# Kernel tuning notes

Hardware: AMD Instinct MI355X
Metric: run time of the kernel (lower is better)

The kernel has to match this reference:

```python
import jax, jax.numpy as jnp
import numpy as np

BRANCH = 8
LEVELS = 7
N = (BRANCH ** LEVELS - 1) // (BRANCH - 1)  # 299593 nodes, complete 8-ary tree
VOCAB, IN_DIM, MEM = 50000, 300, 150


def _tree_structure():
    parent = np.empty(N, np.int32)
    parent[0] = N  # sentinel: root scatters into dropped segment N
    idx = np.arange(1, N)
    parent[1:] = (idx - 1) // BRANCH
    depth = np.empty(N, np.int32)
    start = 0
    for d in range(LEVELS):
        cnt = BRANCH ** d
        depth[start:start + cnt] = d
        start += cnt
    return jnp.asarray(parent), jnp.asarray(depth)


def setup_inputs() -> dict:
    key = jax.random.key(0)
    ks = jax.random.split(key, 20)
    parent, depth = _tree_structure()
    inp = {
        'tokens': jax.random.randint(ks[0], (N,), 0, VOCAB, dtype=jnp.int32),
        'parent': parent,
        'depth': depth,
        'max_depth': LEVELS,
        'emb': jax.random.normal(ks[1], (VOCAB, IN_DIM), jnp.float32) * 0.1,
    }
    names_x = ['Wix', 'Wfx', 'Wox', 'Wux']
    names_h = ['Wih', 'Wfh', 'Woh', 'Wuh']
    sx = 1.0 / np.sqrt(IN_DIM)
    sh = 1.0 / np.sqrt(MEM)
    for j, (nx, nh) in enumerate(zip(names_x, names_h)):
        inp[nx] = jax.random.normal(ks[2 + 4 * j], (MEM, IN_DIM), jnp.float32) * sx
        inp['b' + nx[1:]] = jax.random.normal(ks[3 + 4 * j], (MEM,), jnp.float32) * sx
        inp[nh] = jax.random.normal(ks[4 + 4 * j], (MEM, MEM), jnp.float32) * sh
        inp['b' + nh[1:]] = jax.random.normal(ks[5 + 4 * j], (MEM,), jnp.float32) * sh
    return inp


def reference(tokens, parent, depth, max_depth, emb,
              Wix, bix, Wih, bih, Wfx, bfx, Wfh, bfh,
              Wox, box, Woh, boh, Wux, bux, Wuh, buh):
    n = tokens.shape[0]
    x = emb[tokens]  # [N, in_dim]
    # precompute all input-side gate projections once (batched GEMMs)
    ix_x = x @ Wix.T + bix
    fx_x = x @ Wfx.T + bfx
    ox_x = x @ Wox.T + box
    ux_x = x @ Wux.T + bux
    # parent index safe for gathering (root's sentinel -> 0; its row is masked out)
    gparent = jnp.where(parent >= n, 0, parent)

    h = jnp.zeros((n, MEM), x.dtype)
    c = jnp.zeros((n, MEM), x.dtype)

    # level-synchronous bottom-up sweep (loop over tree depth, not data)
    for d in range(max_depth - 1, -1, -1):
        # per-child forget gate: sigmoid(fh(h_child) + fx(x_parent)) * c_child
        f = jax.nn.sigmoid(h @ Wfh.T + bfh + fx_x[gparent])
        fc_sum = jax.ops.segment_sum(f * c, parent, num_segments=n + 1)[:n]
        h_sum = jax.ops.segment_sum(h, parent, num_segments=n + 1)[:n]
        i = jax.nn.sigmoid(ix_x + h_sum @ Wih.T + bih)
        o = jax.nn.sigmoid(ox_x + h_sum @ Woh.T + boh)
        u = jnp.tanh(ux_x + h_sum @ Wuh.T + buh)
        c_new = i * u + fc_sum
        h_new = o * jnp.tanh(c_new)
        mask = (depth == d)[:, None]
        c = jnp.where(mask, c_new, c)
        h = jnp.where(mask, h_new, h)
    # original returns concatenated cell states (post-order); here indexed by node id
    return c
```

## Files before the change

### kernel.cpp

```cpp
#include <hip/hip_runtime.h>


#define MEMD  150
#define IND   300
#define NINT  37449
#define VOCAB 50000
#define GROW  608
#define FSTR  152

typedef short bf16x8 __attribute__((ext_vector_type(8)));
typedef float f32x16 __attribute__((ext_vector_type(16)));
#define ZERO16 {0,0,0,0,0,0,0,0,0,0,0,0,0,0,0,0}

#define GALL_OFF 0ul
#define HSB_OFF  60800000ul
#define FCS_OFF  72200000ul
#define BPX_OFF  94980000ul
#define BPH_OFF  95380000ul

__device__ __forceinline__ float b2f(unsigned short u) {
    union { unsigned int i; float f; } v; v.i = ((unsigned int)u) << 16; return v.f;
}
__device__ __forceinline__ unsigned short f2b(float f) {
    union { float f; unsigned int i; } v; v.f = f;
    unsigned int x = v.i;
    x += 0x7fffu + ((x >> 16) & 1u);
    return (unsigned short)(x >> 16);
}
__device__ __forceinline__ float sigm(float x) {
    return __builtin_amdgcn_rcpf(1.0f + __expf(-x));
}
__device__ __forceinline__ float tanh_fast(float x) {
    float e = __expf(2.0f * x);
    return 1.0f - 2.0f * __builtin_amdgcn_rcpf(e + 1.0f);
}

__global__ void pack_w(const float* __restrict__ Wix, const float* __restrict__ Wox,
                       const float* __restrict__ Wux, const float* __restrict__ Wfx,
                       const float* __restrict__ Wih, const float* __restrict__ Woh,
                       const float* __restrict__ Wuh, const float* __restrict__ Wfh,
                       unsigned short* __restrict__ bpx, unsigned short* __restrict__ bph)
{
    const int total_x = 4 * 5 * 19 * 512;
    const int total_h = 4 * 5 * 10 * 512;
    for (int i = blockIdx.x * blockDim.x + threadIdx.x; i < total_x + total_h;
         i += gridDim.x * blockDim.x) {
        if (i < total_x) {
            int e = i & 7, lane = (i >> 3) & 63, rest = i >> 9;
            int ks = rest % 19; rest /= 19;
            int nt = rest % 5;  int g = rest / 5;
            int col = nt * 32 + (lane & 31);
            int k = ks * 16 + ((lane >> 5) << 3) + e;
            const float* W = (g == 0) ? Wix : (g == 1) ? Wox : (g == 2) ? Wux : Wfx;
            bpx[i] = f2b((col < MEMD && k < IND) ? W[col * IND + k] : 0.f);
        } else {
            int j = i - total_x;
            int e = j & 7, lane = (j >> 3) & 63, rest = j >> 9;
            int ks = rest % 10; rest /= 10;
            int nt = rest % 5;  int g = rest / 5;
            int col = nt * 32 + (lane & 31);
            int k = ks * 16 + ((lane >> 5) << 3) + e;
            const float* W = (g == 0) ? Wih : (g == 1) ? Woh : (g == 2) ? Wuh : Wfh;
            bph[j] = f2b((col < MEMD && k < MEMD) ? W[col * MEMD + k] : 0.f);
        }
    }
}

__global__ __launch_bounds__(640, 2)
void vocab_gemm(const float* __restrict__ emb,
                const float* __restrict__ bix, const float* __restrict__ bih,
                const float* __restrict__ box_, const float* __restrict__ boh,
                const float* __restrict__ bux, const float* __restrict__ buh,
                const float* __restrict__ bfx, const float* __restrict__ bfh,
                const unsigned short* __restrict__ bpx_u,
                unsigned short* __restrict__ gall)
{
    __shared__ __align__(16) char sm0[40960];
    const int tid = threadIdx.x, lane = tid & 63, w = tid >> 6;
    const int hi = lane >> 5, ln31 = lane & 31;
    const int tile0 = blockIdx.x * 64;
    const int rowsValid = min(64, VOCAB - tile0);
    const int mt = (w >= 5) ? 1 : 0, nt = w - mt * 5;

    for (int i = tid; i < 64 * 40; i += 640) {
        int r = i / 40, q = i % 40;
        int rr = (r < rowsValid) ? r : 0;
        const float* er = emb + (long)(tile0 + rr) * IND;
        float4 v0 = {0.f,0.f,0.f,0.f}, v1 = {0.f,0.f,0.f,0.f};
        if (q < 38) v0 = *(const float4*)(er + q * 8);
        if (q < 37) v1 = *(const float4*)(er + q * 8 + 4);
        bf16x8 p;
        p[0]=(short)f2b(v0.x); p[1]=(short)f2b(v0.y); p[2]=(short)f2b(v0.z); p[3]=(short)f2b(v0.w);
        p[4]=(short)f2b(v1.x); p[5]=(short)f2b(v1.y); p[6]=(short)f2b(v1.z); p[7]=(short)f2b(v1.w);
        *(bf16x8*)(sm0 + r * 640 + ((q * 16) ^ ((r & 7) << 4))) = p;
    }
    __syncthreads();

    const bf16x8* BX = (const bf16x8*)bpx_u;
    const int row = mt * 32 + ln31;
    const int col = nt * 32 + ln31;
    const bool colv = col < MEMD;
    const int cc = colv ? col : 0;
    const float* b1[4] = {bix, box_, bux, bfx};
    const float* b2[4] = {bih, boh, buh, bfh};

    for (int g = 0; g < 4; ++g) {
        f32x16 acc = ZERO16;
        bf16x8 aC = *(const bf16x8*)(sm0 + row * 640 + ((hi * 16) ^ ((row & 7) << 4)));
        bf16x8 bC = BX[((g * 5 + nt) * 19 + 0) * 64 + lane];
        #pragma unroll
        for (int ks = 0; ks < 19; ++ks) {
            bf16x8 aN, bN;
            if (ks < 18) {
                aN = *(const bf16x8*)(sm0 + row * 640 + (((ks + 1) * 32 + hi * 16) ^ ((row & 7) << 4)));
                bN = BX[((g * 5 + nt) * 19 + ks + 1) * 64 + lane];
            }
            acc = __builtin_amdgcn_mfma_f32_32x32x16_bf16(aC, bC, acc, 0, 0, 0);
            aC = aN; bC = bN;
        }
        float bias = colv ? (b1[g][cc] + b2[g][cc]) : 0.f;
        #pragma unroll
        for (int r = 0; r < 16; ++r) {
            int rloc = mt * 32 + (r & 3) + 8 * (r >> 2) + 4 * hi;
            if (rloc < rowsValid && colv)
                gall[(long)(tile0 + rloc) * GROW + col * 4 + g] = f2b(acc[r] + bias);
        }
    }
}

template<bool INTERNAL>
__global__ __launch_bounds__(320, INTERNAL ? 2 : 8)
void level_k(const int* __restrict__ tokens,
             const unsigned short* __restrict__ gall,
             const unsigned short* __restrict__ bph_u,
             unsigned short* __restrict__ hsumb, unsigned short* __restrict__ fcsum,
             float* __restrict__ c_out, int base, int cnt, int writePar)
{
    __shared__ __align__(16) char sm0[INTERNAL ? 24576 : 12288];
    __shared__ int toksL[32];
    __shared__ int ptokL[4];
    const int tid = threadIdx.x, lane = tid & 63, w = tid >> 6;
    const int hi = lane >> 5, ln31 = lane & 31;
    const int tile0 = blockIdx.x * 32;
    const int nodeBase = base + tile0;
    const int rowsValid = INTERNAL ? min(32, cnt - tile0) : 32;
    const int p0 = (nodeBase - 1) >> 3;
    const int nt = w;

    if (tid < 32) toksL[tid] = tokens[nodeBase + ((tid < rowsValid) ? tid : 0)];
    if (writePar && tid < 4) ptokL[tid] = tokens[p0 + tid];
    if (INTERNAL) {
        for (int i = tid; i < 32 * 20; i += 320) {
            int r = i / 20, q = i % 20;
            int rr = (r < rowsValid) ? r : 0;
            bf16x8 v = {0,0,0,0,0,0,0,0};
            if (q < 19)
                v = *(const bf16x8*)(hsumb + (long)(nodeBase + rr) * FSTR + q * 8);
            *(bf16x8*)(sm0 + 12288 + r * 384 + ((q * 16) ^ ((r & 7) << 4))) = v;
        }
    }
    __syncthreads();

    const bf16x8* BH = (const bf16x8*)bph_u;
    const int row = ln31;
    const int col = nt * 32 + ln31;
    const bool colv = col < MEMD;
    const int cc = colv ? col : 0;

    f32x16 ai = ZERO16, ao = ZERO16, au = ZERO16;
    if (INTERNAL) {
        const char* hb = sm0 + 12288;
        bf16x8 aC = *(const bf16x8*)(hb + row * 384 + ((hi * 16) ^ ((row & 7) << 4)));
        bf16x8 b0C = BH[((0 * 5 + nt) * 10 + 0) * 64 + lane];
        bf16x8 b1C = BH[((1 * 5 + nt) * 10 + 0) * 64 + lane];
        bf16x8 b2C = BH[((2 * 5 + nt) * 10 + 0) * 64 + lane];
        #pragma unroll
        for (int ks = 0; ks < 10; ++ks) {
            bf16x8 aN, b0N, b1N, b2N;
            if (ks < 9) {
                aN  = *(const bf16x8*)(hb + row * 384 + (((ks + 1) * 32 + hi * 16) ^ ((row & 7) << 4)));
                b0N = BH[((0 * 5 + nt) * 10 + ks + 1) * 64 + lane];
                b1N = BH[((1 * 5 + nt) * 10 + ks + 1) * 64 + lane];
                b2N = BH[((2 * 5 + nt) * 10 + ks + 1) * 64 + lane];
            }
            ai = __builtin_amdgcn_mfma_f32_32x32x16_bf16(aC, b0C, ai, 0, 0, 0);
            ao = __builtin_amdgcn_mfma_f32_32x32x16_bf16(aC, b1C, ao, 0, 0, 0);
            au = __builtin_amdgcn_mfma_f32_32x32x16_bf16(aC, b2C, au, 0, 0, 0);
            aC = aN; b0C = b0N; b1C = b1N; b2C = b2N;
        }
    }

    float cvv[16];
    {
        float hp[4] = {0.f, 0.f, 0.f, 0.f};
        #pragma unroll
        for (int r = 0; r < 16; ++r) {
            int rloc = (r & 3) + 8 * (r >> 2) + 4 * hi;
            bool rv = INTERNAL ? (rloc < rowsValid) : true;
            ushort4 gv = *(const ushort4*)(gall + (long)toksL[rloc] * GROW + cc * 4);
            float fc = 0.f;
            if (INTERNAL) fc = (rv && colv) ? b2f(fcsum[(long)(nodeBase + rloc) * FSTR + col]) : 0.f;
            float iv = sigm((INTERNAL ? ai[r] : 0.f) + b2f(gv.x));
            float ov = sigm((INTERNAL ? ao[r] : 0.f) + b2f(gv.y));
            float uv = tanh_fast((INTERNAL ? au[r] : 0.f) + b2f(gv.z));
            float cv = iv * uv + fc;
            float h = (rv && colv) ? ov * tanh_fast(cv) : 0.f;
            cvv[r] = (rv && colv) ? cv : 0.f;
            if (rv && colv) c_out[(long)(nodeBase + rloc) * MEMD + col] = cv;
            *(unsigned short*)(sm0 + rloc * 384 + ((col * 2) ^ ((rloc & 7) << 4))) = f2b(h);
            hp[r >> 2] += h;
        }
        if (writePar) {
            #pragma unroll
            for (int o = 0; o < 4; ++o) {
                float s = hp[o] + __shfl_xor(hp[o], 32);
                if (lane < 32 && colv && (INTERNAL ? (o * 8 < rowsValid) : true))
                    hsumb[(long)(p0 + o) * FSTR + col] = f2b(s);
            }
        }
    }
    __syncthreads();

    if (writePar) {
        f32x16 ff = ZERO16;
        {
            bf16x8 aC = *(const bf16x8*)(sm0 + row * 384 + ((hi * 16) ^ ((row & 7) << 4)));
            bf16x8 bC = BH[((15 + nt) * 10 + 0) * 64 + lane];
            #pragma unroll
            for (int ks = 0; ks < 10; ++ks) {
                bf16x8 aN, bN;
                if (ks < 9) {
                    aN = *(const bf16x8*)(sm0 + row * 384 + (((ks + 1) * 32 + hi * 16) ^ ((row & 7) << 4)));
                    bN = BH[((15 + nt) * 10 + ks + 1) * 64 + lane];
                }
                ff = __builtin_amdgcn_mfma_f32_32x32x16_bf16(aC, bC, ff, 0, 0, 0);
                aC = aN; bC = bN;
            }
        }
        #pragma unroll
        for (int o = 0; o < 4; ++o) {
            float fx = b2f(gall[(long)ptokL[o] * GROW + cc * 4 + 3]);
            float fp = 0.f;
            #pragma unroll
            for (int q = 0; q < 4; ++q) {
                int r = o * 4 + q;
                fp += sigm(ff[r] + fx) * cvv[r];
            }
            float s = fp + __shfl_xor(fp, 32);
            if (lane < 32 && colv && (INTERNAL ? (o * 8 < rowsValid) : true))
                fcsum[(long)(p0 + o) * FSTR + col] = f2b(s);
        }
    }
}

__global__ __launch_bounds__(320, 2)
void tail_k(const int* __restrict__ tokens,
            const unsigned short* __restrict__ gall,
            const unsigned short* __restrict__ bph_u,
            unsigned short* __restrict__ hsumb, unsigned short* __restrict__ fcsum,
            float* __restrict__ c_out)
{
    __shared__ __align__(16) char sm0[24576];
    __shared__ int toksL[32];
    __shared__ int ptokL[4];
    const int tid = threadIdx.x, lane = tid & 63, w = tid >> 6;
    const int hi = lane >> 5, ln31 = lane & 31;
    const int nt = w;
    const bf16x8* BH = (const bf16x8*)bph_u;
    const int row = ln31;
    const int col = nt * 32 + ln31;
    const bool colv = col < MEMD;
    const int cc = colv ? col : 0;

    const int basesL[3] = {9, 1, 0};
    const int cntsL[3]  = {64, 8, 1};
    const int wpL[3]    = {1, 1, 0};

    for (int li = 0; li < 3; ++li) {
        for (int t0 = 0; t0 < cntsL[li]; t0 += 32) {
            const int nodeBase = basesL[li] + t0;
            const int rowsValid = min(32, cntsL[li] - t0);
            const int p0 = (nodeBase - 1) >> 3;
            const int writePar = wpL[li];

            if (tid < 32) toksL[tid] = tokens[nodeBase + ((tid < rowsValid) ? tid : 0)];
            if (writePar && tid < 4) ptokL[tid] = tokens[p0 + tid];
            for (int i = tid; i < 32 * 20; i += 320) {
                int r = i / 20, q = i % 20;
                int rr = (r < rowsValid) ? r : 0;
                bf16x8 v = {0,0,0,0,0,0,0,0};
                if (q < 19)
                    v = *(const bf16x8*)(hsumb + (long)(nodeBase + rr) * FSTR + q * 8);
                *(bf16x8*)(sm0 + 12288 + r * 384 + ((q * 16) ^ ((r & 7) << 4))) = v;
            }
            __syncthreads();

            f32x16 ai = ZERO16, ao = ZERO16, au = ZERO16;
            {
                const char* hb = sm0 + 12288;
                #pragma unroll
                for (int ks = 0; ks < 10; ++ks) {
                    bf16x8 a = *(const bf16x8*)(hb + row * 384 + ((ks * 32 + hi * 16) ^ ((row & 7) << 4)));
                    ai = __builtin_amdgcn_mfma_f32_32x32x16_bf16(a, BH[((0 * 5 + nt) * 10 + ks) * 64 + lane], ai, 0, 0, 0);
                    ao = __builtin_amdgcn_mfma_f32_32x32x16_bf16(a, BH[((1 * 5 + nt) * 10 + ks) * 64 + lane], ao, 0, 0, 0);
                    au = __builtin_amdgcn_mfma_f32_32x32x16_bf16(a, BH[((2 * 5 + nt) * 10 + ks) * 64 + lane], au, 0, 0, 0);
                }
            }

            float cvv[16];
            {
                float hp[4] = {0.f, 0.f, 0.f, 0.f};
                #pragma unroll
                for (int r = 0; r < 16; ++r) {
                    int rloc = (r & 3) + 8 * (r >> 2) + 4 * hi;
                    bool rv = rloc < rowsValid;
                    ushort4 gv = *(const ushort4*)(gall + (long)toksL[rloc] * GROW + cc * 4);
                    float fc = (rv && colv) ? b2f(fcsum[(long)(nodeBase + rloc) * FSTR + col]) : 0.f;
                    float iv = sigm(ai[r] + b2f(gv.x));
                    float ov = sigm(ao[r] + b2f(gv.y));
                    float uv = tanh_fast(au[r] + b2f(gv.z));
                    float cv = iv * uv + fc;
                    float h = (rv && colv) ? ov * tanh_fast(cv) : 0.f;
                    cvv[r] = (rv && colv) ? cv : 0.f;
                    if (rv && colv) c_out[(long)(nodeBase + rloc) * MEMD + col] = cv;
                    *(unsigned short*)(sm0 + rloc * 384 + ((col * 2) ^ ((rloc & 7) << 4))) = f2b(h);
                    hp[r >> 2] += h;
                }
                if (writePar) {
                    #pragma unroll
                    for (int o = 0; o < 4; ++o) {
                        float s = hp[o] + __shfl_xor(hp[o], 32);
                        if (lane < 32 && colv && o * 8 < rowsValid)
                            hsumb[(long)(p0 + o) * FSTR + col] = f2b(s);
                    }
                }
            }
            __syncthreads();

            if (writePar) {
                f32x16 ff = ZERO16;
                #pragma unroll
                for (int ks = 0; ks < 10; ++ks) {
                    bf16x8 a = *(const bf16x8*)(sm0 + row * 384 + ((ks * 32 + hi * 16) ^ ((row & 7) << 4)));
                    ff = __builtin_amdgcn_mfma_f32_32x32x16_bf16(a, BH[((15 + nt) * 10 + ks) * 64 + lane], ff, 0, 0, 0);
                }
                #pragma unroll
                for (int o = 0; o < 4; ++o) {
                    float fx = b2f(gall[(long)ptokL[o] * GROW + cc * 4 + 3]);
                    float fp = 0.f;
                    #pragma unroll
                    for (int q = 0; q < 4; ++q)
                        fp += sigm(ff[o * 4 + q] + fx) * cvv[o * 4 + q];
                    float s = fp + __shfl_xor(fp, 32);
                    if (lane < 32 && colv && o * 8 < rowsValid)
                        fcsum[(long)(p0 + o) * FSTR + col] = f2b(s);
                }
            }
            __syncthreads();
        }
    }
}

extern "C" void kernel_launch(void* const* d_in, const int* in_sizes, int n_in,
                              void* d_out, int out_size, void* d_ws, size_t ws_size,
                              hipStream_t stream) {
    const int*   tokens = (const int*)d_in[0];
    const float* emb = (const float*)d_in[4];
    const float* Wix = (const float*)d_in[5];  const float* bix = (const float*)d_in[6];
    const float* Wih = (const float*)d_in[7];  const float* bih = (const float*)d_in[8];
    const float* Wfx = (const float*)d_in[9];  const float* bfx = (const float*)d_in[10];
    const float* Wfh = (const float*)d_in[11]; const float* bfh = (const float*)d_in[12];
    const float* Wox = (const float*)d_in[13]; const float* box_ = (const float*)d_in[14];
    const float* Woh = (const float*)d_in[15]; const float* boh = (const float*)d_in[16];
    const float* Wux = (const float*)d_in[17]; const float* bux = (const float*)d_in[18];
    const float* Wuh = (const float*)d_in[19]; const float* buh = (const float*)d_in[20];
    float* c_out = (float*)d_out;
    char* ws = (char*)d_ws;

    unsigned short* gall  = (unsigned short*)(ws + GALL_OFF);
    unsigned short* hsumb = (unsigned short*)(ws + HSB_OFF);
    unsigned short* fcs   = (unsigned short*)(ws + FCS_OFF);
    unsigned short* bpx   = (unsigned short*)(ws + BPX_OFF);
    unsigned short* bph   = (unsigned short*)(ws + BPH_OFF);

    pack_w<<<128, 512, 0, stream>>>(Wix, Wox, Wux, Wfx, Wih, Woh, Wuh, Wfh, bpx, bph);
    vocab_gemm<<<(VOCAB + 63) / 64, 640, 0, stream>>>(
        emb, bix, bih, box_, boh, bux, buh, bfx, bfh, bpx, gall);

    static const int bases[7] = {0, 1, 9, 73, 585, 4681, 37449};
    static const int cnts[7]  = {1, 8, 64, 512, 4096, 32768, 262144};

    level_k<false><<<cnts[6] / 32, 320, 0, stream>>>(
        tokens, gall, bph, hsumb, fcs, c_out, bases[6], cnts[6], 1);
    for (int d = 5; d >= 3; --d) {
        int grid = (cnts[d] + 31) / 32;
        level_k<true><<<grid, 320, 0, stream>>>(
            tokens, gall, bph, hsumb, fcs, c_out, bases[d], cnts[d], 1);
    }
    tail_k<<<1, 320, 0, stream>>>(tokens, gall, bph, hsumb, fcs, c_out);
}
```

Baseline: 302.9 us.

## Precompute leaf hidden states and forget projections per vocab token

Leaf nodes depend only on their token, so leaf h and the Wfh·h projection are computed once per vocabulary entry (50000 rows) rather than per leaf node (262144). They are stored in an fp8 e4m3 table and gathered by a new leaf_csum kernel that reduces the eight children per parent. This removes the per-leaf MFMA GEMM but adds two extra kernels plus fp8 quantisation error in the forget-gate input. Gall stride shrinks from 608 to 600.

```diff
diff --git a/kernel.cpp b/kernel.cpp
--- a/kernel.cpp
+++ b/kernel.cpp
@@ -5,7 +5,7 @@
 #define IND   300
 #define NINT  37449
 #define VOCAB 50000
-#define GROW  608
+#define GROW  600
 #define FSTR  152
 
 typedef short bf16x8 __attribute__((ext_vector_type(8)));
@@ -13,10 +13,11 @@
 #define ZERO16 {0,0,0,0,0,0,0,0,0,0,0,0,0,0,0,0}
 
 #define GALL_OFF 0ul
-#define HSB_OFF  60800000ul
-#define FCS_OFF  72200000ul
-#define BPX_OFF  94980000ul
-#define BPH_OFF  95380000ul
+#define FHX_OFF  60000000ul
+#define HSB_OFF  67600000ul
+#define FCS_OFF  79000000ul
+#define BPX_OFF  90400000ul
+#define BPH_OFF  90800000ul
 
 __device__ __forceinline__ float b2f(unsigned short u) {
     union { unsigned int i; float f; } v; v.i = ((unsigned int)u) << 16; return v.f;
@@ -33,6 +34,34 @@
 __device__ __forceinline__ float tanh_fast(float x) {
     float e = __expf(2.0f * x);
     return 1.0f - 2.0f * __builtin_amdgcn_rcpf(e + 1.0f);
+}
+__device__ __forceinline__ unsigned char f2e4m3(float f) {
+    union { float f; unsigned u; } v; v.f = f;
+    unsigned s = (v.u >> 31) << 7;
+    float af = fabsf(f);
+    if (af >= 448.f) return (unsigned char)(s | 0x7E);
+    if (af < 0.015625f) {
+        int m = (int)(af * 512.f + 0.5f);
+        if (m > 7) m = 7;
+        return (unsigned char)(s | m);
+    }
+    unsigned u = v.u & 0x7fffffffu;
+    u += 0x7ffffu + ((u >> 20) & 1u);
+    int ef = (int)(u >> 23) - 120;
+    unsigned m = (u >> 20) & 7u;
+    if (ef < 1) { ef = 1; m = 0; }
+    if (ef > 15) { ef = 15; m = 6; }
+    return (unsigned char)(s | (ef << 3) | m);
+}
+__device__ __forceinline__ float e4m3f(unsigned char u) {
+    unsigned s = (u >> 7) & 1u, ef = (u >> 3) & 15u, m = u & 7u;
+    if (ef == 0) {
+        float r = (float)m * 0.001953125f;
+        return s ? -r : r;
+    }
+    union { unsigned u; float f; } v;
+    v.u = (s << 31) | ((ef + 120) << 23) | (m << 20);
+    return v.f;
 }
 
 __global__ void pack_w(const float* __restrict__ Wix, const float* __restrict__ Wox,
@@ -128,36 +157,134 @@
     }
 }
 
-template<bool INTERNAL>
-__global__ __launch_bounds__(320, INTERNAL ? 2 : 8)
+__global__ __launch_bounds__(256, 8)
+void hleaf_k(const unsigned short* __restrict__ gall, unsigned short* __restrict__ htmp)
+{
+    int i = blockIdx.x * 256 + threadIdx.x;
+    if (i >= VOCAB * FSTR) return;
+    int v = i / FSTR, col = i % FSTR;
+    unsigned short r = 0;
+    if (col < MEMD) {
+        ushort4 gv = *(const ushort4*)(gall + (long)v * GROW + col * 4);
+        float iv = sigm(b2f(gv.x));
+        float ov = sigm(b2f(gv.y));
+        float uv = tanh_fast(b2f(gv.z));
+        float cv = iv * uv;
+        r = f2b(ov * tanh_fast(cv));
+    }
+    htmp[i] = r;
+}
+
+__global__ __launch_bounds__(320, 4)
+void fhx_gemm(const unsigned short* __restrict__ htmp,
+              const unsigned short* __restrict__ bph_u,
+              unsigned char* __restrict__ fhx)
+{
+    __shared__ __align__(16) char sm0[12288];
+    const int tid = threadIdx.x, lane = tid & 63, w = tid >> 6;
+    const int hi = lane >> 5, ln31 = lane & 31;
+    const int tile0 = blockIdx.x * 32;
+    const int rowsValid = min(32, VOCAB - tile0);
+    const int nt = w;
+
+    for (int i = tid; i < 32 * 20; i += 320) {
+        int r = i / 20, q = i % 20;
+        int rr = (r < rowsValid) ? r : 0;
+        bf16x8 v = {0,0,0,0,0,0,0,0};
+        if (q < 19) v = *(const bf16x8*)(htmp + (long)(tile0 + rr) * FSTR + q * 8);
+        *(bf16x8*)(sm0 + r * 384 + ((q * 16) ^ ((r & 7) << 4))) = v;
+    }
+    __syncthreads();
+
+    const bf16x8* BH = (const bf16x8*)bph_u;
+    const int row = ln31;
+    f32x16 ff = ZERO16;
+    #pragma unroll
+    for (int ks = 0; ks < 10; ++ks) {
+        bf16x8 a = *(const bf16x8*)(sm0 + row * 384 + ((ks * 32 + hi * 16) ^ ((row & 7) << 4)));
+        ff = __builtin_amdgcn_mfma_f32_32x32x16_bf16(a, BH[((15 + nt) * 10 + ks) * 64 + lane], ff, 0, 0, 0);
+    }
+    const int col = nt * 32 + ln31;
+    if (col < MEMD) {
+        #pragma unroll
+        for (int r = 0; r < 16; ++r) {
+            int rloc = (r & 3) + 8 * (r >> 2) + 4 * hi;
+            if (rloc < rowsValid)
+                fhx[(long)(tile0 + rloc) * FSTR + col] = f2e4m3(ff[r]);
+        }
+    }
+}
+
+__global__ __launch_bounds__(320, 8)
+void leaf_csum(const int* __restrict__ tokens,
+               const unsigned short* __restrict__ gall,
+               const unsigned char* __restrict__ fhx,
+               unsigned short* __restrict__ hsumb, unsigned short* __restrict__ fcs,
+               float* __restrict__ c_out)
+{
+    __shared__ int ctok[16];
+    __shared__ int ptokL[2];
+    const int tid = threadIdx.x;
+    const int pl = tid / 160;
+    const int col0 = tid % 160;
+    const bool colv = col0 < MEMD;
+    const int col = colv ? col0 : (MEMD - 1);
+    const int pidx = blockIdx.x * 2 + pl;
+    const int pnode = 4681 + pidx;
+    const long cbase = 8L * pnode + 1;
+    if (tid < 16) ctok[tid] = tokens[37449 + blockIdx.x * 16 + tid];
+    if (tid < 2)  ptokL[tid] = tokens[4681 + blockIdx.x * 2 + tid];
+    __syncthreads();
+
+    const float fxp = b2f(gall[(long)ptokL[pl] * GROW + col * 4 + 3]);
+    float hs = 0.f, fc = 0.f;
+    #pragma unroll
+    for (int k = 0; k < 8; ++k) {
+        int ct = ctok[pl * 8 + k];
+        ushort4 gv = *(const ushort4*)(gall + (long)ct * GROW + col * 4);
+        float iv = sigm(b2f(gv.x));
+        float ov = sigm(b2f(gv.y));
+        float uv = tanh_fast(b2f(gv.z));
+        float cv = iv * uv;
+        float h = ov * tanh_fast(cv);
+        float f = sigm(e4m3f(fhx[(long)ct * FSTR + col]) + fxp);
+        hs += h;
+        fc += f * cv;
+        if (colv) c_out[(cbase + k) * MEMD + col] = cv;
+    }
+    if (colv) {
+        hsumb[(long)pnode * FSTR + col] = f2b(hs);
+        fcs[(long)pnode * FSTR + col]  = f2b(fc);
+    }
+}
+
+__global__ __launch_bounds__(320, 2)
 void level_k(const int* __restrict__ tokens,
              const unsigned short* __restrict__ gall,
              const unsigned short* __restrict__ bph_u,
              unsigned short* __restrict__ hsumb, unsigned short* __restrict__ fcsum,
              float* __restrict__ c_out, int base, int cnt, int writePar)
 {
-    __shared__ __align__(16) char sm0[INTERNAL ? 24576 : 12288];
+    __shared__ __align__(16) char sm0[24576];
     __shared__ int toksL[32];
     __shared__ int ptokL[4];
     const int tid = threadIdx.x, lane = tid & 63, w = tid >> 6;
     const int hi = lane >> 5, ln31 = lane & 31;
     const int tile0 = blockIdx.x * 32;
     const int nodeBase = base + tile0;
-    const int rowsValid = INTERNAL ? min(32, cnt - tile0) : 32;
+    const int rowsValid = min(32, cnt - tile0);
     const int p0 = (nodeBase - 1) >> 3;
     const int nt = w;
 
     if (tid < 32) toksL[tid] = tokens[nodeBase + ((tid < rowsValid) ? tid : 0)];
     if (writePar && tid < 4) ptokL[tid] = tokens[p0 + tid];
-    if (INTERNAL) {
-        for (int i = tid; i < 32 * 20; i += 320) {
-            int r = i / 20, q = i % 20;
-            int rr = (r < rowsValid) ? r : 0;
-            bf16x8 v = {0,0,0,0,0,0,0,0};
-            if (q < 19)
-                v = *(const bf16x8*)(hsumb + (long)(nodeBase + rr) * FSTR + q * 8);
-            *(bf16x8*)(sm0 + 12288 + r * 384 + ((q * 16) ^ ((r & 7) << 4))) = v;
-        }
+    for (int i = tid; i < 32 * 20; i += 320) {
+        int r = i / 20, q = i % 20;
+        int rr = (r < rowsValid) ? r : 0;
+        bf16x8 v = {0,0,0,0,0,0,0,0};
+        if (q < 19)
+            v = *(const bf16x8*)(hsumb + (long)(nodeBase + rr) * FSTR + q * 8);
+        *(bf16x8*)(sm0 + 12288 + r * 384 + ((q * 16) ^ ((r & 7) << 4))) = v;
     }
     __syncthreads();
 
@@ -168,7 +295,7 @@
     const int cc = colv ? col : 0;
 
     f32x16 ai = ZERO16, ao = ZERO16, au = ZERO16;
-    if (INTERNAL) {
+    {
         const char* hb = sm0 + 12288;
         bf16x8 aC = *(const bf16x8*)(hb + row * 384 + ((hi * 16) ^ ((row & 7) << 4)));
         bf16x8 b0C = BH[((0 * 5 + nt) * 10 + 0) * 64 + lane];
@@ -196,14 +323,13 @@
         #pragma unroll
         for (int r = 0; r < 16; ++r) {
             int rloc = (r & 3) + 8 * (r >> 2) + 4 * hi;
-            bool rv = INTERNAL ? (rloc < rowsValid) : true;
+            bool rv = rloc < rowsValid;
             ushort4 gv = *(const ushort4*)(gall + (long)toksL[rloc] * GROW + cc * 4);
-            float fc = 0.f;
-            if (INTERNAL) fc = (rv && colv) ? b2f(fcsum[(long)(nodeBase + rloc) * FSTR + col]) : 0.f;
-            float iv = sigm((INTERNAL ? ai[r] : 0.f) + b2f(gv.x));
-            float ov = sigm((INTERNAL ? ao[r] : 0.f) + b2f(gv.y));
-            float uv = tanh_fast((INTERNAL ? au[r] : 0.f) + b2f(gv.z));
-            float cv = iv * uv + fc;
+            float fcin = (rv && colv) ? b2f(fcsum[(long)(nodeBase + rloc) * FSTR + col]) : 0.f;
+            float iv = sigm(ai[r] + b2f(gv.x));
+            float ov = sigm(ao[r] + b2f(gv.y));
+            float uv = tanh_fast(au[r] + b2f(gv.z));
+            float cv = iv * uv + fcin;
             float h = (rv && colv) ? ov * tanh_fast(cv) : 0.f;
             cvv[r] = (rv && colv) ? cv : 0.f;
             if (rv && colv) c_out[(long)(nodeBase + rloc) * MEMD + col] = cv;
@@ -214,7 +340,7 @@
             #pragma unroll
             for (int o = 0; o < 4; ++o) {
                 float s = hp[o] + __shfl_xor(hp[o], 32);
-                if (lane < 32 && colv && (INTERNAL ? (o * 8 < rowsValid) : true))
+                if (lane < 32 && colv && o * 8 < rowsValid)
                     hsumb[(long)(p0 + o) * FSTR + col] = f2b(s);
             }
         }
@@ -247,7 +373,7 @@
                 fp += sigm(ff[r] + fx) * cvv[r];
             }
             float s = fp + __shfl_xor(fp, 32);
-            if (lane < 32 && colv && (INTERNAL ? (o * 8 < rowsValid) : true))
+            if (lane < 32 && colv && o * 8 < rowsValid)
                 fcsum[(long)(p0 + o) * FSTR + col] = f2b(s);
         }
     }
@@ -315,11 +441,11 @@
                     int rloc = (r & 3) + 8 * (r >> 2) + 4 * hi;
                     bool rv = rloc < rowsValid;
                     ushort4 gv = *(const ushort4*)(gall + (long)toksL[rloc] * GROW + cc * 4);
-                    float fc = (rv && colv) ? b2f(fcsum[(long)(nodeBase + rloc) * FSTR + col]) : 0.f;
+                    float fcin = (rv && colv) ? b2f(fcsum[(long)(nodeBase + rloc) * FSTR + col]) : 0.f;
                     float iv = sigm(ai[r] + b2f(gv.x));
                     float ov = sigm(ao[r] + b2f(gv.y));
                     float uv = tanh_fast(au[r] + b2f(gv.z));
-                    float cv = iv * uv + fc;
+                    float cv = iv * uv + fcin;
                     float h = (rv && colv) ? ov * tanh_fast(cv) : 0.f;
                     cvv[r] = (rv && colv) ? cv : 0.f;
                     if (rv && colv) c_out[(long)(nodeBase + rloc) * MEMD + col] = cv;
@@ -378,7 +504,9 @@
     char* ws = (char*)d_ws;
 
     unsigned short* gall  = (unsigned short*)(ws + GALL_OFF);
+    unsigned char*  fhx   = (unsigned char*)(ws + FHX_OFF);
     unsigned short* hsumb = (unsigned short*)(ws + HSB_OFF);
+    unsigned short* htmp  = (unsigned short*)(ws + HSB_OFF);
     unsigned short* fcs   = (unsigned short*)(ws + FCS_OFF);
     unsigned short* bpx   = (unsigned short*)(ws + BPX_OFF);
     unsigned short* bph   = (unsigned short*)(ws + BPH_OFF);
@@ -386,15 +514,15 @@
     pack_w<<<128, 512, 0, stream>>>(Wix, Wox, Wux, Wfx, Wih, Woh, Wuh, Wfh, bpx, bph);
     vocab_gemm<<<(VOCAB + 63) / 64, 640, 0, stream>>>(
         emb, bix, bih, box_, boh, bux, buh, bfx, bfh, bpx, gall);
+    hleaf_k<<<(VOCAB * FSTR + 255) / 256, 256, 0, stream>>>(gall, htmp);
+    fhx_gemm<<<(VOCAB + 31) / 32, 320, 0, stream>>>(htmp, bph, fhx);
+    leaf_csum<<<16384, 320, 0, stream>>>(tokens, gall, fhx, hsumb, fcs, c_out);
 
     static const int bases[7] = {0, 1, 9, 73, 585, 4681, 37449};
     static const int cnts[7]  = {1, 8, 64, 512, 4096, 32768, 262144};
-
-    level_k<false><<<cnts[6] / 32, 320, 0, stream>>>(
-        tokens, gall, bph, hsumb, fcs, c_out, bases[6], cnts[6], 1);
     for (int d = 5; d >= 3; --d) {
         int grid = (cnts[d] + 31) / 32;
-        level_k<true><<<grid, 320, 0, stream>>>(
+        level_k<<<grid, 320, 0, stream>>>(
             tokens, gall, bph, hsumb, fcs, c_out, bases[d], cnts[d], 1);
     }
     tail_k<<<1, 320, 0, stream>>>(tokens, gall, bph, hsumb, fcs, c_out);
```

Measured after the change: 332.7 us. 1.1x slower.
